# Performance work log

Hardware: AMD Instinct MI355X
Metric: run time of the kernel (lower is better)

The kernel has to match this reference:

```python
import jax, jax.numpy as jnp
import numpy as np


def _conv1x1(x, W, b):
    # 1x1 conv == per-pixel channel matmul: x [B,C,H,W], W [O,C], b [O]
    return jnp.einsum('bchw,oc->bohw', x, W) + b[None, :, None, None]


def setup_inputs() -> dict:
    key = jax.random.key(0)
    ks = jax.random.split(key, 9)
    B, C, H, W = 16, 512, 32, 32
    s = 1.0 / np.sqrt(C)
    inp = {
        'x': jax.random.normal(ks[0], (B, C, H, W), dtype=jnp.float32),
        'Wq': jax.random.normal(ks[1], (C, C), dtype=jnp.float32) * s,
        'bq': jax.random.normal(ks[2], (C,), dtype=jnp.float32) * 0.01,
        'Wk': jax.random.normal(ks[3], (C, C), dtype=jnp.float32) * s,
        'bk': jax.random.normal(ks[4], (C,), dtype=jnp.float32) * 0.01,
        'Wv': jax.random.normal(ks[5], (C, C), dtype=jnp.float32) * s,
        'bv': jax.random.normal(ks[6], (C,), dtype=jnp.float32) * 0.01,
        'Wo': jax.random.normal(ks[7], (C, C), dtype=jnp.float32) * s,
        'bo': jax.random.normal(ks[8], (C,), dtype=jnp.float32) * 0.01,
    }
    return inp


def reference(x, Wq, bq, Wk, bk, Wv, bv, Wo, bo):
    B, C, H, W = x.shape
    q = _conv1x1(x, Wq, bq)
    k = _conv1x1(x, Wk, bk)
    v = _conv1x1(x, Wv, bv)
    hw = H * W
    qf = q.reshape(B, C, hw)  # [B,C,HW]
    kf = k.reshape(B, C, hw)
    vf = v.reshape(B, C, hw)
    # scores[b,i,j] = sum_c q[b,c,i] * k[b,c,j], scaled by c^-0.5
    scores = jnp.einsum('bci,bcj->bij', qf, kf) * (C ** -0.5)
    attn = jax.nn.softmax(scores, axis=2)  # softmax over keys j
    # out[b,c,i] = sum_j v[b,c,j] * attn[b,i,j]
    out = jnp.einsum('bcj,bij->bci', vf, attn).reshape(B, C, H, W)
    out = _conv1x1(out, Wo, bo)
    return x + out
```

## Files before the change

kernel.cpp:

```cpp
#include <hip/hip_runtime.h>
#include <hip/hip_bf16.h>
#include <math.h>


typedef __bf16 bf16x8 __attribute__((ext_vector_type(8)));
typedef float  f32x4  __attribute__((ext_vector_type(4)));

__device__ __forceinline__ unsigned short f2bf(float f) {
    unsigned u = __float_as_uint(f);
    u += 0x7fff + ((u >> 16) & 1);
    return (unsigned short)(u >> 16);
}

__device__ __forceinline__ void gload_lds16(const void* g, void* l) {
    __builtin_amdgcn_global_load_lds(
        (const __attribute__((address_space(1))) void*)g,
        (__attribute__((address_space(3))) void*)l, 16, 0, 0);
}

template<int N> __device__ __forceinline__ void waitcnt_vm() {
    if constexpr (N == 0) asm volatile("s_waitcnt vmcnt(0)" ::: "memory");
    else if constexpr (N == 3) asm volatile("s_waitcnt vmcnt(3)" ::: "memory");
    else if constexpr (N == 4) asm volatile("s_waitcnt vmcnt(4)" ::: "memory");
    else if constexpr (N == 6) asm volatile("s_waitcnt vmcnt(6)" ::: "memory");
    else if constexpr (N == 8) asm volatile("s_waitcnt vmcnt(8)" ::: "memory");
}

struct GemmP {
    const unsigned short* A;
    const unsigned short* B;
    void* C;
    const float* bias;
    const float* resid;
    int M, N, K, ldA, ldB;
    long sA, sB, sC, sR;
    float scale;
};

template<int MT, int NT, bool OUT_F32, int BIAS_MODE, bool RESID, int EXPM>
__device__ __forceinline__ void gemm_body(const GemmP p, int L,
                                          unsigned short* Als,
                                          unsigned short* Bls)
{
    constexpr int BM   = MT * 32;
    constexpr int BN   = NT * 64;
    constexpr int APAN = BM * 32;
    constexpr int BPAN = BN * 32;
    constexpr int ACH  = BM / 128;
    constexpr int BCH  = BN / 128;
    constexpr int LPS  = ACH + BCH;

    const int xcd = L & 7;
    const int idx = L >> 3;
    const int bz  = xcd * 2 + (idx >> 4);
    const int w   = idx & 15;
    const int m0  = (w >> 2) * BM;
    const int n0  = (w & 3) * BN;

    const unsigned short* A = p.A + bz * p.sA;
    const unsigned short* B = p.B + bz * p.sB;

    const int tid  = threadIdx.x;
    const int lane = tid & 63;
    const int wave = tid >> 6;
    const int wm   = wave >> 2;
    const int wn   = wave & 3;

    const int ar = lane >> 2;
    const int ak = ((lane & 3) ^ ((ar >> 1) & 3)) * 8;

    const unsigned short* agp = A + (long)(m0 + wave * 16 + ar) * p.ldA + ak;
    const unsigned short* bgp = B + (long)(n0 + wave * 16 + ar) * p.ldB + ak;
    const long aj = 128L * p.ldA;
    const long bj = 128L * p.ldB;

    const int fr = lane & 15;
    const int fq = lane >> 4;
    const int kph = (fq ^ ((fr >> 1) & 3)) * 8;

    f32x4 acc[MT][NT] = {};
    f32x4 acc1[MT] = {};
    bf16x8 ones;
    if constexpr (EXPM == 2) {
        #pragma unroll
        for (int i = 0; i < 8; ++i) ones[i] = (__bf16)1.0f;
    }

    const int nsteps = p.K >> 5;

    auto STAGE = [&](int sel) {
        unsigned short* a0 = Als + sel * APAN;
        unsigned short* b0 = Bls + sel * BPAN;
        gload_lds16(agp, a0 + wave * 512);
        if constexpr (ACH == 2) gload_lds16(agp + aj, a0 + (wave + 8) * 512);
        gload_lds16(bgp, b0 + wave * 512);
        if constexpr (BCH == 2) gload_lds16(bgp + bj, b0 + (wave + 8) * 512);
        agp += 32; bgp += 32;
    };

    auto COMPUTE = [&](int sel) {
        const unsigned short* Ap = Als + sel * APAN;
        const unsigned short* Bp = Bls + sel * BPAN;
        bf16x8 af[MT], bfr[NT];
        #pragma unroll
        for (int mt = 0; mt < MT; ++mt)
            af[mt] = *(const bf16x8*)&Ap[(wm * MT * 16 + mt * 16 + fr) * 32 + kph];
        #pragma unroll
        for (int nt = 0; nt < NT; ++nt)
            bfr[nt] = *(const bf16x8*)&Bp[(wn * NT * 16 + nt * 16 + fr) * 32 + kph];
        __builtin_amdgcn_s_setprio(1);
        if constexpr (EXPM == 2) {
            #pragma unroll
            for (int mt = 0; mt < MT; ++mt)
                acc1[mt] = __builtin_amdgcn_mfma_f32_16x16x32_bf16(
                    af[mt], ones, acc1[mt], 0, 0, 0);
        }
        #pragma unroll
        for (int mt = 0; mt < MT; ++mt)
            #pragma unroll
            for (int nt = 0; nt < NT; ++nt)
                acc[mt][nt] = __builtin_amdgcn_mfma_f32_16x16x32_bf16(
                    af[mt], bfr[nt], acc[mt][nt], 0, 0, 0);
        __builtin_amdgcn_s_setprio(0);
    };

    STAGE(0); STAGE(1); STAGE(2);

    for (int t = 0; t < nsteps - 2; ++t) {
        __builtin_amdgcn_sched_barrier(0);
        waitcnt_vm<2 * LPS>();
        __builtin_amdgcn_s_barrier();
        asm volatile("" ::: "memory");
        __builtin_amdgcn_sched_barrier(0);
        if (t + 3 < nsteps) STAGE((t + 3) & 3);
        COMPUTE(t & 3);
    }
    __builtin_amdgcn_sched_barrier(0);
    waitcnt_vm<LPS>();
    __builtin_amdgcn_s_barrier();
    asm volatile("" ::: "memory");
    __builtin_amdgcn_sched_barrier(0);
    COMPUTE((nsteps - 2) & 3);
    __builtin_amdgcn_sched_barrier(0);
    waitcnt_vm<0>();
    __builtin_amdgcn_s_barrier();
    asm volatile("" ::: "memory");
    __builtin_amdgcn_sched_barrier(0);
    COMPUTE((nsteps - 1) & 3);

    float* Cf = (float*)p.C + bz * p.sC;
    unsigned short* Ch = (unsigned short*)p.C + bz * p.sC;
    const float* resid = RESID ? (p.resid + bz * p.sR) : nullptr;
    const int N = p.N;

    if constexpr (EXPM == 1) {
        #pragma unroll
        for (int mt = 0; mt < MT; ++mt)
            #pragma unroll
            for (int r = 0; r < 4; ++r) {
                const int row = m0 + wm * MT * 16 + mt * 16 + fq * 4 + r;
                #pragma unroll
                for (int nt = 0; nt < NT; ++nt) {
                    const int col = n0 + wn * NT * 16 + nt * 16 + fr;
                    Ch[(long)row * N + col] = f2bf(__expf(acc[mt][nt][r] * p.scale));
                }
            }
    } else {
        #pragma unroll
        for (int mt = 0; mt < MT; ++mt) {
            float linv[4];
            if constexpr (EXPM == 2) {
                #pragma unroll
                for (int r = 0; r < 4; ++r)
                    linv[r] = 1.0f / acc1[mt][r];
            }
            #pragma unroll
            for (int nt = 0; nt < NT; ++nt) {
                const int col = n0 + wn * NT * 16 + nt * 16 + fr;
                const float bn2 = (BIAS_MODE == 2) ? p.bias[col] : 0.0f;
                #pragma unroll
                for (int r = 0; r < 4; ++r) {
                    const int row = m0 + wm * MT * 16 + mt * 16 + fq * 4 + r;
                    float val = acc[mt][nt][r] + bn2;
                    if (BIAS_MODE == 1) val += p.bias[row];
                    if constexpr (EXPM == 2) val *= linv[r];
                    const long o = (long)row * N + col;
                    if (RESID) val += resid[o];
                    if (OUT_F32) Cf[o] = val;
                    else         Ch[o] = f2bf(val);
                }
            }
        }
    }
}

template<int MT, int NT, bool OUT_F32, int BIAS_MODE, bool RESID, int EXPM>
__global__ __launch_bounds__(512, 2) void gemm_k(GemmP p)
{
    __shared__ unsigned short Als[4 * MT * 1024];
    __shared__ unsigned short Bls[4 * NT * 2048];
    gemm_body<MT, NT, OUT_F32, BIAS_MODE, RESID, EXPM>(p, blockIdx.x, Als, Bls);
}

__global__ __launch_bounds__(512, 2) void gemm_qkv_fused(GemmP pqk, GemmP pv)
{
    __shared__ unsigned short LDS[65536];
    if ((int)blockIdx.x < 256)
        gemm_body<8, 4, false, 2, false, 0>(pqk, blockIdx.x,
                                            LDS, LDS + 4 * 8 * 1024);
    else
        gemm_body<4, 4, false, 1, false, 0>(pv, blockIdx.x - 256,
                                            LDS, LDS + 4 * 4 * 1024);
}

__global__ __launch_bounds__(256) void prep_all(
    const float* __restrict__ x, unsigned short* __restrict__ xT,
    const float* __restrict__ Wq, const float* __restrict__ Wk,
    const float* __restrict__ Wv, const float* __restrict__ Wo,
    const float* __restrict__ bq, const float* __restrict__ bk,
    unsigned short* __restrict__ Wb, float* __restrict__ biasqk)
{
    const int b = blockIdx.x;
    const int t = threadIdx.x;
    if (b < 2048) {
        __shared__ unsigned short tlb[64 * 64];
        const int batch = b >> 7;
        const int rem = b & 127;
        const int c0 = (rem >> 4) * 64;
        const int p0 = (rem & 15) * 64;
        const float* xb = x + (long)batch * 524288;
        unsigned short* xTb = xT + (long)batch * 524288;
        const int lx = t & 15;
        const int ly = t >> 4;
        #pragma unroll
        for (int i = 0; i < 4; ++i) {
            const int c = ly + 16 * i;
            const float4 f = *(const float4*)&xb[(long)(c0 + c) * 1024 + p0 + lx * 4];
            ushort4 h;
            h.x = f2bf(f.x); h.y = f2bf(f.y); h.z = f2bf(f.z); h.w = f2bf(f.w);
            const int colp = (lx * 4) ^ (((c >> 3) & 7) << 3);
            *(ushort4*)&tlb[c * 64 + colp] = h;
        }
        __syncthreads();
        const int sx = t & 7;
        const int sy = t >> 3;
        #pragma unroll
        for (int i = 0; i < 2; ++i) {
            const int r = sy + 32 * i;
            ushort4 lo, hi;
            lo.x = tlb[(sx * 8 + 0) * 64 + (r ^ (sx << 3))];
            lo.y = tlb[(sx * 8 + 1) * 64 + (r ^ (sx << 3))];
            lo.z = tlb[(sx * 8 + 2) * 64 + (r ^ (sx << 3))];
            lo.w = tlb[(sx * 8 + 3) * 64 + (r ^ (sx << 3))];
            hi.x = tlb[(sx * 8 + 4) * 64 + (r ^ (sx << 3))];
            hi.y = tlb[(sx * 8 + 5) * 64 + (r ^ (sx << 3))];
            hi.z = tlb[(sx * 8 + 6) * 64 + (r ^ (sx << 3))];
            hi.w = tlb[(sx * 8 + 7) * 64 + (r ^ (sx << 3))];
            unsigned short* o = &xTb[(long)(p0 + r) * 512 + c0 + sx * 8];
            *(ushort4*)o = lo;
            *(ushort4*)(o + 4) = hi;
        }
    } else if (b < 3072) {
        const int wb = b - 2048;
        const float* srcs[4] = {Wq, Wk, Wv, Wo};
        const float* s = srcs[wb >> 8];
        unsigned short* d = Wb + (long)(wb >> 8) * 262144;
        const int i = ((wb & 255) * 256 + t) * 4;
        const float4 f = *(const float4*)(s + i);
        ushort4 h;
        h.x = f2bf(f.x); h.y = f2bf(f.y); h.z = f2bf(f.z); h.w = f2bf(f.w);
        *(ushort4*)(d + i) = h;
    } else {
        biasqk[t]       = bq[t];
        biasqk[256 + t] = bq[256 + t];
        biasqk[512 + t] = bk[t];
        biasqk[768 + t] = bk[256 + t];
    }
}

extern "C" void kernel_launch(void* const* d_in, const int* in_sizes, int n_in,
                              void* d_out, int out_size, void* d_ws, size_t ws_size,
                              hipStream_t stream)
{
    const float* x  = (const float*)d_in[0];
    const float* Wq = (const float*)d_in[1];
    const float* bq = (const float*)d_in[2];
    const float* Wk = (const float*)d_in[3];
    const float* bk = (const float*)d_in[4];
    const float* Wv = (const float*)d_in[5];
    const float* bv = (const float*)d_in[6];
    const float* Wo = (const float*)d_in[7];
    const float* bo = (const float*)d_in[8];
    float* out = (float*)d_out;

    const int C = 512, HW = 1024;
    const int Bn = 16;
    const long CHW = (long)C * HW;
    const long SHW = (long)HW * HW;

    unsigned short* xT   = (unsigned short*)d_ws;
    unsigned short* qkT  = xT + Bn * CHW;
    unsigned short* vB   = qkT + Bn * SHW;
    unsigned short* expS = vB + Bn * CHW;
    unsigned short* Wb   = expS + Bn * SHW;
    float* biasqk = (float*)(Wb + 4 * 262144);
    unsigned short* OT = xT;

    unsigned short* Wvb = Wb + 2 * 262144;
    unsigned short* Wob = Wb + 3 * 262144;

    const float scale = 0.044194173824159216f;

    prep_all<<<dim3(3073), dim3(256), 0, stream>>>(x, xT, Wq, Wk, Wv, Wo,
                                                   bq, bk, Wb, biasqk);

    GemmP pqk = { xT, Wb, qkT, biasqk, nullptr,
                  HW, 2 * C, C, C, C, CHW, 0, SHW, 0, 0.0f };
    GemmP pv  = { Wvb, xT, vB, bv, nullptr,
                  C, HW, C, C, C, 0, CHW, CHW, 0, 0.0f };
    gemm_qkv_fused<<<dim3(512), dim3(512), 0, stream>>>(pqk, pv);

    GemmP ps  = { qkT, qkT + C, expS, nullptr, nullptr,
                  HW, HW, C, 2 * C, 2 * C, SHW, SHW, SHW, 0, scale };
    gemm_k<8, 4, false, 0, false, 1><<<dim3(256), dim3(512), 0, stream>>>(ps);

    GemmP po  = { expS, vB, OT, nullptr, nullptr,
                  HW, C, HW, HW, HW, SHW, CHW, CHW, 0, 0.0f };
    gemm_k<8, 2, false, 0, false, 2><<<dim3(256), dim3(512), 0, stream>>>(po);

    GemmP pout = { Wob, OT, out, bo, x,
                   C, HW, C, C, C, 0, CHW, CHW, CHW, 0.0f };
    gemm_k<4, 4, true, 1, true, 0><<<dim3(256), dim3(512), 0, stream>>>(pout);
}
```

Baseline: 219.4 us.

## Merge all stages into one persistent kernel with software grid barriers

Replaces the chain of five launches (prep, fused QKV, scores, PV, output projection) with a single persistent 256-block kernel. Stages are separated by atomic-counter grid barriers, and a tiny init kernel resets the counters. The goal is to remove per-launch overhead and tail gaps between kernels. In exchange, QKV now runs the qk and v GEMMs back to back in each block rather than as 512 concurrent blocks. The barrier relies on all 256 blocks being co-resident, with no cooperative-launch guarantee, so it could deadlock if they are not.

```diff
diff --git a/kernel.cpp b/kernel.cpp
--- a/kernel.cpp
+++ b/kernel.cpp
@@ -194,88 +194,114 @@
     }
 }
 
-template<int MT, int NT, bool OUT_F32, int BIAS_MODE, bool RESID, int EXPM>
-__global__ __launch_bounds__(512, 2) void gemm_k(GemmP p)
-{
-    __shared__ unsigned short Als[4 * MT * 1024];
-    __shared__ unsigned short Bls[4 * NT * 2048];
-    gemm_body<MT, NT, OUT_F32, BIAS_MODE, RESID, EXPM>(p, blockIdx.x, Als, Bls);
-}
-
-__global__ __launch_bounds__(512, 2) void gemm_qkv_fused(GemmP pqk, GemmP pv)
+__device__ __forceinline__ void grid_bar(unsigned* cnt)
+{
+    __syncthreads();
+    __threadfence();
+    if (threadIdx.x == 0) {
+        __hip_atomic_fetch_add(cnt, 1u, __ATOMIC_ACQ_REL, __HIP_MEMORY_SCOPE_AGENT);
+        while (__hip_atomic_load(cnt, __ATOMIC_ACQUIRE, __HIP_MEMORY_SCOPE_AGENT) < 256u)
+            __builtin_amdgcn_s_sleep(2);
+    }
+    __syncthreads();
+    __threadfence();
+}
+
+struct MegaP {
+    GemmP pqk, pv, ps, po, pout;
+    const float *x, *Wq, *Wk, *Wv, *Wo, *bq, *bk;
+    unsigned short *xT, *Wb;
+    float *biasqk;
+    unsigned *bar;
+};
+
+__global__ void init_bar(unsigned* bar)
+{
+    if (threadIdx.x < 8) bar[threadIdx.x] = 0u;
+}
+
+__global__ __launch_bounds__(512) void mega(MegaP P)
 {
     __shared__ unsigned short LDS[65536];
-    if ((int)blockIdx.x < 256)
-        gemm_body<8, 4, false, 2, false, 0>(pqk, blockIdx.x,
-                                            LDS, LDS + 4 * 8 * 1024);
-    else
-        gemm_body<4, 4, false, 1, false, 0>(pv, blockIdx.x - 256,
-                                            LDS, LDS + 4 * 4 * 1024);
-}
-
-__global__ __launch_bounds__(256) void prep_all(
-    const float* __restrict__ x, unsigned short* __restrict__ xT,
-    const float* __restrict__ Wq, const float* __restrict__ Wk,
-    const float* __restrict__ Wv, const float* __restrict__ Wo,
-    const float* __restrict__ bq, const float* __restrict__ bk,
-    unsigned short* __restrict__ Wb, float* __restrict__ biasqk)
-{
-    const int b = blockIdx.x;
-    const int t = threadIdx.x;
-    if (b < 2048) {
-        __shared__ unsigned short tlb[64 * 64];
-        const int batch = b >> 7;
-        const int rem = b & 127;
-        const int c0 = (rem >> 4) * 64;
-        const int p0 = (rem & 15) * 64;
-        const float* xb = x + (long)batch * 524288;
-        unsigned short* xTb = xT + (long)batch * 524288;
-        const int lx = t & 15;
-        const int ly = t >> 4;
-        #pragma unroll
-        for (int i = 0; i < 4; ++i) {
-            const int c = ly + 16 * i;
-            const float4 f = *(const float4*)&xb[(long)(c0 + c) * 1024 + p0 + lx * 4];
+    const int b   = blockIdx.x;
+    const int tid = threadIdx.x;
+
+    {
+        const int team = tid >> 8;
+        const int t    = tid & 255;
+        unsigned short* tlb = LDS + team * 4096;
+        #pragma unroll
+        for (int r0 = 0; r0 < 4; ++r0) {
+            const int job   = b * 8 + r0 * 2 + team;
+            const int batch = job >> 7;
+            const int rem   = job & 127;
+            const int c0 = (rem >> 4) * 64;
+            const int p0 = (rem & 15) * 64;
+            const float* xb = P.x + (long)batch * 524288;
+            unsigned short* xTb = P.xT + (long)batch * 524288;
+            const int lx = t & 15;
+            const int ly = t >> 4;
+            #pragma unroll
+            for (int i = 0; i < 4; ++i) {
+                const int c = ly + 16 * i;
+                const float4 f = *(const float4*)&xb[(long)(c0 + c) * 1024 + p0 + lx * 4];
+                ushort4 h;
+                h.x = f2bf(f.x); h.y = f2bf(f.y); h.z = f2bf(f.z); h.w = f2bf(f.w);
+                const int colp = (lx * 4) ^ (((c >> 3) & 7) << 3);
+                *(ushort4*)&tlb[c * 64 + colp] = h;
+            }
+            __syncthreads();
+            const int sx = t & 7;
+            const int sy = t >> 3;
+            #pragma unroll
+            for (int i = 0; i < 2; ++i) {
+                const int r = sy + 32 * i;
+                ushort4 lo, hi;
+                lo.x = tlb[(sx * 8 + 0) * 64 + (r ^ (sx << 3))];
+                lo.y = tlb[(sx * 8 + 1) * 64 + (r ^ (sx << 3))];
+                lo.z = tlb[(sx * 8 + 2) * 64 + (r ^ (sx << 3))];
+                lo.w = tlb[(sx * 8 + 3) * 64 + (r ^ (sx << 3))];
+                hi.x = tlb[(sx * 8 + 4) * 64 + (r ^ (sx << 3))];
+                hi.y = tlb[(sx * 8 + 5) * 64 + (r ^ (sx << 3))];
+                hi.z = tlb[(sx * 8 + 6) * 64 + (r ^ (sx << 3))];
+                hi.w = tlb[(sx * 8 + 7) * 64 + (r ^ (sx << 3))];
+                unsigned short* o = &xTb[(long)(p0 + r) * 512 + c0 + sx * 8];
+                *(ushort4*)o = lo;
+                *(ushort4*)(o + 4) = hi;
+            }
+            __syncthreads();
+        }
+        for (int i = b * 512 + tid; i < 262144; i += 131072) {
+            const int mat = i >> 16;
+            const int off = (i & 65535) * 4;
+            const float* s = (mat == 0) ? P.Wq : (mat == 1) ? P.Wk
+                           : (mat == 2) ? P.Wv : P.Wo;
+            const float4 f = *(const float4*)(s + off);
             ushort4 h;
             h.x = f2bf(f.x); h.y = f2bf(f.y); h.z = f2bf(f.z); h.w = f2bf(f.w);
-            const int colp = (lx * 4) ^ (((c >> 3) & 7) << 3);
-            *(ushort4*)&tlb[c * 64 + colp] = h;
-        }
-        __syncthreads();
-        const int sx = t & 7;
-        const int sy = t >> 3;
-        #pragma unroll
-        for (int i = 0; i < 2; ++i) {
-            const int r = sy + 32 * i;
-            ushort4 lo, hi;
-            lo.x = tlb[(sx * 8 + 0) * 64 + (r ^ (sx << 3))];
-            lo.y = tlb[(sx * 8 + 1) * 64 + (r ^ (sx << 3))];
-            lo.z = tlb[(sx * 8 + 2) * 64 + (r ^ (sx << 3))];
-            lo.w = tlb[(sx * 8 + 3) * 64 + (r ^ (sx << 3))];
-            hi.x = tlb[(sx * 8 + 4) * 64 + (r ^ (sx << 3))];
-            hi.y = tlb[(sx * 8 + 5) * 64 + (r ^ (sx << 3))];
-            hi.z = tlb[(sx * 8 + 6) * 64 + (r ^ (sx << 3))];
-            hi.w = tlb[(sx * 8 + 7) * 64 + (r ^ (sx << 3))];
-            unsigned short* o = &xTb[(long)(p0 + r) * 512 + c0 + sx * 8];
-            *(ushort4*)o = lo;
-            *(ushort4*)(o + 4) = hi;
-        }
-    } else if (b < 3072) {
-        const int wb = b - 2048;
-        const float* srcs[4] = {Wq, Wk, Wv, Wo};
-        const float* s = srcs[wb >> 8];
-        unsigned short* d = Wb + (long)(wb >> 8) * 262144;
-        const int i = ((wb & 255) * 256 + t) * 4;
-        const float4 f = *(const float4*)(s + i);
-        ushort4 h;
-        h.x = f2bf(f.x); h.y = f2bf(f.y); h.z = f2bf(f.z); h.w = f2bf(f.w);
-        *(ushort4*)(d + i) = h;
-    } else {
-        biasqk[t]       = bq[t];
-        biasqk[256 + t] = bq[256 + t];
-        biasqk[512 + t] = bk[t];
-        biasqk[768 + t] = bk[256 + t];
-    }
+            *(ushort4*)(P.Wb + (long)mat * 262144 + off) = h;
+        }
+        if (b == 0 && tid < 256) {
+            P.biasqk[tid]       = P.bq[tid];
+            P.biasqk[256 + tid] = P.bq[256 + tid];
+            P.biasqk[512 + tid] = P.bk[tid];
+            P.biasqk[768 + tid] = P.bk[256 + tid];
+        }
+    }
+    grid_bar(P.bar + 0);
+
+    gemm_body<8, 4, false, 2, false, 0>(P.pqk, b, LDS, LDS + 32768);
+    __syncthreads();
+    gemm_body<4, 4, false, 1, false, 0>(P.pv, b, LDS, LDS + 16384);
+    grid_bar(P.bar + 1);
+
+    gemm_body<8, 4, false, 0, false, 1>(P.ps, b, LDS, LDS + 32768);
+    grid_bar(P.bar + 2);
+
+    gemm_body<8, 2, false, 0, false, 2>(P.po, b, LDS, LDS + 32768);
+    grid_bar(P.bar + 3);
+
+    gemm_body<4, 4, true, 1, true, 0>(P.pout, b, LDS, LDS + 16384);
 }
 
 extern "C" void kernel_launch(void* const* d_in, const int* in_sizes, int n_in,
@@ -304,6 +330,7 @@
     unsigned short* expS = vB + Bn * CHW;
     unsigned short* Wb   = expS + Bn * SHW;
     float* biasqk = (float*)(Wb + 4 * 262144);
+    unsigned* bar = (unsigned*)(biasqk + 1024);
     unsigned short* OT = xT;
 
     unsigned short* Wvb = Wb + 2 * 262144;
@@ -311,24 +338,21 @@
 
     const float scale = 0.044194173824159216f;
 
-    prep_all<<<dim3(3073), dim3(256), 0, stream>>>(x, xT, Wq, Wk, Wv, Wo,
-                                                   bq, bk, Wb, biasqk);
-
-    GemmP pqk = { xT, Wb, qkT, biasqk, nullptr,
-                  HW, 2 * C, C, C, C, CHW, 0, SHW, 0, 0.0f };
-    GemmP pv  = { Wvb, xT, vB, bv, nullptr,
-                  C, HW, C, C, C, 0, CHW, CHW, 0, 0.0f };
-    gemm_qkv_fused<<<dim3(512), dim3(512), 0, stream>>>(pqk, pv);
-
-    GemmP ps  = { qkT, qkT + C, expS, nullptr, nullptr,
-                  HW, HW, C, 2 * C, 2 * C, SHW, SHW, SHW, 0, scale };
-    gemm_k<8, 4, false, 0, false, 1><<<dim3(256), dim3(512), 0, stream>>>(ps);
-
-    GemmP po  = { expS, vB, OT, nullptr, nullptr,
-                  HW, C, HW, HW, HW, SHW, CHW, CHW, 0, 0.0f };
-    gemm_k<8, 2, false, 0, false, 2><<<dim3(256), dim3(512), 0, stream>>>(po);
-
-    GemmP pout = { Wob, OT, out, bo, x,
-                   C, HW, C, C, C, 0, CHW, CHW, CHW, 0.0f };
-    gemm_k<4, 4, true, 1, true, 0><<<dim3(256), dim3(512), 0, stream>>>(pout);
-}
+    MegaP mp;
+    mp.pqk = { xT, Wb, qkT, biasqk, nullptr,
+               HW, 2 * C, C, C, C, CHW, 0, SHW, 0, 0.0f };
+    mp.pv  = { Wvb, xT, vB, bv, nullptr,
+               C, HW, C, C, C, 0, CHW, CHW, 0, 0.0f };
+    mp.ps  = { qkT, qkT + C, expS, nullptr, nullptr,
+               HW, HW, C, 2 * C, 2 * C, SHW, SHW, SHW, 0, scale };
+    mp.po  = { expS, vB, OT, nullptr, nullptr,
+               HW, C, HW, HW, HW, SHW, CHW, CHW, 0, 0.0f };
+    mp.pout = { Wob, OT, out, bo, x,
+                C, HW, C, C, C, 0, CHW, CHW, CHW, 0.0f };
+    mp.x = x; mp.Wq = Wq; mp.Wk = Wk; mp.Wv = Wv; mp.Wo = Wo;
+    mp.bq = bq; mp.bk = bk;
+    mp.xT = xT; mp.Wb = Wb; mp.biasqk = biasqk; mp.bar = bar;
+
+    init_bar<<<dim3(1), dim3(64), 0, stream>>>(bar);
+    mega<<<dim3(256), dim3(512), 0, stream>>>(mp);
+}
```

After: 570.4 us. +160.0%, slower.
